# Optimization experiments

Hardware: AMD Instinct MI355X
Metric: run time of the kernel (lower is better)

## Reference

```python
import jax, jax.numpy as jnp
import numpy as np
import math

B, N, E_PER = 128, 512, 2048
D = 16
NUM_REL = 114
NUM_ATTR = 10
LAYERS = 3
RATIO = 0.8
TN = B * N
TE = B * E_PER
NEG_SLOPE = 0.2


def setup_inputs() -> dict:
    key = jax.random.key(0)
    ks = jax.random.split(key, 16)
    x_attr = jax.random.randint(ks[0], (TN,), 0, NUM_ATTR, dtype=jnp.int32)
    # edges constrained within each graph's contiguous block of N nodes
    src = jax.random.randint(ks[1], (B, E_PER), 0, N, dtype=jnp.int32)
    dst = jax.random.randint(ks[2], (B, E_PER), 0, N, dtype=jnp.int32)
    off = (jnp.arange(B, dtype=jnp.int32) * N)[:, None]
    edge_index = jnp.stack([(src + off).reshape(-1), (dst + off).reshape(-1)])
    edge_type = jax.random.randint(ks[3], (TE,), 0, NUM_REL, dtype=jnp.int32)
    emb = jax.random.normal(ks[4], (NUM_ATTR, D)) * 0.3
    gnn_w = jax.random.normal(ks[5], (LAYERS, NUM_REL, D, D)) * (1.0 / np.sqrt(D))
    gnn_q = jax.random.normal(ks[6], (LAYERS, D, 1)) * 0.3
    gnn_k = jax.random.normal(ks[7], (LAYERS, D, 1)) * 0.3
    gnn_b = jnp.zeros((LAYERS, D))
    pool_w = jax.random.normal(ks[8], (LAYERS - 1, D)) * 0.3
    w1 = jax.random.normal(ks[9], (D * LAYERS * 2, 16)) * (1.0 / np.sqrt(D * LAYERS * 2))
    b1 = jnp.zeros((16,))
    w2 = jax.random.normal(ks[10], (16, 4)) * 0.25
    b2 = jnp.zeros((4,))
    w3 = jax.random.normal(ks[11], (4, 1)) * 0.5
    b3 = jnp.zeros((1,))
    return dict(emb=emb, gnn_w=gnn_w, gnn_q=gnn_q, gnn_k=gnn_k, gnn_b=gnn_b,
                pool_w=pool_w, w1=w1, b1=b1, w2=w2, b2=b2, w3=w3, b3=b3,
                x_attr=x_attr, edge_index=edge_index, edge_type=edge_type)


def _rgat_layer(x, src, dst, etype, edge_mask, node_mask, W, q, k, b):
    # PyG RGATConv: heads=1, dim=1, additive-self-attention, across-relation softmax, sum aggr
    w_e = W[etype]                                   # [E, D, D] per-relation gather
    h_s = jnp.einsum('ed,edo->eo', x[src], w_e)      # transformed source (x_j)
    h_t = jnp.einsum('ed,edo->eo', x[dst], w_e)      # transformed target (x_i)
    logit = jax.nn.leaky_relu((h_t @ q + h_s @ k)[:, 0], NEG_SLOPE)  # [E]
    # masked segment softmax over incoming edges of each target node
    m = jax.ops.segment_max(jnp.where(edge_mask, logit, -jnp.inf), dst, num_segments=TN)
    m_e = m[dst]
    ex = jnp.where(edge_mask, jnp.exp(logit - jnp.where(jnp.isfinite(m_e), m_e, 0.0)), 0.0)
    den = jax.ops.segment_sum(ex, dst, num_segments=TN)[dst]
    alpha = ex / jnp.where(den > 0, den, 1.0)
    out = jax.ops.segment_sum(alpha[:, None] * h_s, dst, num_segments=TN) + b
    return jnp.where(node_mask[:, None], jax.nn.relu(out), 0.0)


def reference(emb, gnn_w, gnn_q, gnn_k, gnn_b, pool_w, w1, b1, w2, b2, w3, b3,
              x_attr, edge_index, edge_type):
    src, dst = edge_index[0], edge_index[1]
    x = emb[x_attr]                                  # [TN, D]
    node_mask = jnp.ones((TN,), bool)
    edge_mask = jnp.ones((TE,), bool)
    feats = []
    alive = N
    for l in range(LAYERS):
        x = _rgat_layer(x, src, dst, edge_type, edge_mask, node_mask,
                        gnn_w[l], gnn_q[l], gnn_k[l], gnn_b[l])
        xb = x.reshape(B, N, D)
        mb = node_mask.reshape(B, N)
        cnt = mb.sum(1).astype(x.dtype)[:, None]
        feats.append(xb.sum(1) / cnt)                               # global mean pool
        feats.append(jnp.where(mb[:, :, None], xb, -jnp.inf).max(1))  # global max pool
        if l < LAYERS - 1:
            kk = math.ceil(RATIO * alive)            # static per-graph keep count
            pw = pool_w[l]
            score = jnp.tanh((x @ pw) / jnp.linalg.norm(pw))        # [TN]
            sm = jnp.where(node_mask, score, -jnp.inf).reshape(B, N)
            _, idx = jax.lax.top_k(sm, kk)
            nm = jnp.zeros((B, N), bool).at[jnp.arange(B)[:, None], idx].set(True).reshape(-1)
            x = jnp.where(nm[:, None], x * score[:, None], 0.0)
            node_mask = nm
            edge_mask = edge_mask & nm[src] & nm[dst]
            alive = kk
    g = jnp.concatenate(feats, axis=1)               # [B, 96]
    g = jax.nn.relu(g @ w1 + b1)
    g = jax.nn.relu(g @ w2 + b2)
    return jax.nn.sigmoid(g @ w3 + b3)               # [B, 1]
```

## Files before the change

### kernel.cpp

```cpp
#include <hip/hip_runtime.h>

#define B_ 128
#define NPG 512
#define EPG 2048
#define NREL 114
#define XS 18

__device__ __forceinline__ unsigned fkey(float f){
  unsigned u = __float_as_uint(f);
  return (u & 0x80000000u) ? ~u : (u | 0x80000000u);
}
__device__ __forceinline__ float fdec(unsigned k){
  return (k & 0x80000000u) ? __uint_as_float(k & 0x7FFFFFFFu) : __uint_as_float(~k);
}
__device__ __forceinline__ float dot4f(float4 a, float4 b){
  return a.x*b.x + a.y*b.y + a.z*b.z + a.w*b.w;
}

__device__ __forceinline__ void scan512(int* s_hist, int* s_off, int* s_wt, int tid){
  int lane = tid & 63, wv = tid >> 6;
  int cnt = 0, inc = 0;
  if (wv < 8){
    cnt = s_hist[wv*64 + lane];
    inc = cnt;
    #pragma unroll
    for (int o=1; o<64; o<<=1){ int t=__shfl_up(inc,o); if (lane>=o) inc += t; }
    if (lane==63) s_wt[wv] = inc;
  }
  __syncthreads();
  if (tid < 8){
    int e = 0;
    #pragma unroll
    for (int j=0;j<8;j++) if (j<tid) e += s_wt[j];
    s_wt[8+tid] = e;
  }
  __syncthreads();
  if (wv < 8){
    int base = s_wt[8+wv];
    s_off[wv*64+lane+1] = base + inc;
    s_hist[wv*64+lane]  = base + inc - cnt;
  }
  if (tid==0) s_off[0] = 0;
}

__global__ __launch_bounds__(1024, 4) void k_fused(
    const float* __restrict__ emb, const float* __restrict__ gnn_w,
    const float* __restrict__ gnn_q, const float* __restrict__ gnn_k,
    const float* __restrict__ gnn_b, const float* __restrict__ pool_w,
    const float* __restrict__ w1, const float* __restrict__ b1,
    const float* __restrict__ w2, const float* __restrict__ b2,
    const float* __restrict__ w3, const float* __restrict__ b3,
    const int* __restrict__ xattr, const int* __restrict__ src,
    const int* __restrict__ dst, const int* __restrict__ et,
    float* __restrict__ out)
{
  __shared__ float s_x[NPG*XS];
  __shared__ float s_wq[NREL*XS];
  __shared__ float s_wk[NREL*XS];
  __shared__ unsigned s_epk[EPG+2];
  __shared__ unsigned short s_edst[EPG];
  __shared__ int s_off[NPG+1];
  __shared__ int s_hist[NPG];
  __shared__ unsigned s_keys[NPG];
  __shared__ int s_mask[NPG];
  __shared__ unsigned short s_perm[NPG];
  __shared__ int s_dh[64];
  __shared__ int s_wt[16];
  __shared__ float s_sum[16];
  __shared__ unsigned s_max16[16];
  __shared__ int s_w[16];
  __shared__ float s_feats[96];
  __shared__ float s_h1[16], s_h2[4];

  const int b = blockIdx.x, tid = threadIdx.x;
  const int lane = tid & 63, wv = tid >> 6;
  const int og = tid & 3, grp = tid >> 2;
  const int nb = b*NPG;
  const size_t gb = (size_t)b*EPG;

  if (tid < NPG){
    int a = xattr[nb + tid];
    const float2* e2 = (const float2*)(emb + a*16);
    #pragma unroll
    for (int c=0;c<8;c++) *(float2*)&s_x[tid*XS + 2*c] = e2[c];
    s_mask[tid] = 1;
  }
  for (int i=tid;i<NPG;i+=1024) s_hist[i]=0;
  if (tid<64) s_dh[tid]=0;
  if (tid<2) s_epk[EPG+tid]=0;
  __syncthreads();
  for (int e=tid;e<EPG;e+=1024) atomicAdd(&s_hist[dst[gb+e]-nb], 1);
  __syncthreads();
  scan512(s_hist, s_off, s_wt, tid);
  __syncthreads();
  {
    for (int e=tid;e<EPG;e+=1024){
      int d = dst[gb+e]-nb;
      int p = atomicAdd(&s_hist[d], 1);
      s_epk[p]  = (unsigned)(src[gb+e]-nb) | ((unsigned)et[gb+e]<<16);
      s_edst[p] = (unsigned short)d;
    }
    int mydeg = 0;
    if (tid<NPG){
      mydeg = s_off[tid+1]-s_off[tid]; if (mydeg>63) mydeg=63;
      atomicAdd(&s_dh[mydeg], 1);
    }
    __syncthreads();
    if (tid<64){
      int c = s_dh[tid], inc = c;
      #pragma unroll
      for (int o=1;o<64;o<<=1){ int t=__shfl_up(inc,o); if (tid>=o) inc+=t; }
      s_dh[tid] = inc - c;
    }
    __syncthreads();
    if (tid<NPG){ int p = atomicAdd(&s_dh[mydeg],1); s_perm[p]=(unsigned short)tid; }
  }
  __syncthreads();

  const int cnts[3] = {512, 410, 328};
  const int kks[2]  = {410, 328};

  for (int l=0; l<3; ++l){
    const float* Wl = gnn_w + (size_t)l*NREL*256;
    {
      const float4* q4=(const float4*)(gnn_q+l*16);
      const float4* k4=(const float4*)(gnn_k+l*16);
      float4 q0=q4[0],q1=q4[1],q2=q4[2],q3=q4[3];
      float4 c0=k4[0],c1=k4[1],c2=k4[2],c3=k4[3];
      for (int i=tid;i<NREL*16;i+=1024){
        const float4* wr=(const float4*)(Wl+(size_t)i*16);
        float4 a0=wr[0],a1=wr[1],a2=wr[2],a3=wr[3];
        s_wq[(i>>4)*XS+(i&15)] = dot4f(a0,q0)+dot4f(a1,q1)+dot4f(a2,q2)+dot4f(a3,q3);
        s_wk[(i>>4)*XS+(i&15)] = dot4f(a0,c0)+dot4f(a1,c1)+dot4f(a2,c2)+dot4f(a3,c3);
      }
      if (tid<16){ s_sum[tid]=0.f; s_max16[tid]=0u; }
    }
    __syncthreads();
    float rnorm=0.f; float pw4[4]={0,0,0,0};
    if (l<2){
      float ss=0.f;
      #pragma unroll
      for (int o=0;o<16;o++){ float p=pool_w[l*16+o]; ss+=p*p; }
      rnorm = rsqrtf(ss);
      #pragma unroll
      for (int j=0;j<4;j++) pw4[j]=pool_w[l*16+4*og+j];
    }
    const float* bb = gnn_b + l*16;
    const int nA = s_perm[grp], nB = s_perm[511-grp];
    float zA[4], zB[4];
    auto pm_round = [&](int n, float* z){
      int beg = s_off[n], end = s_off[n+1];
      int alive = s_mask[n];
      float2 xt0 = *(const float2*)&s_x[n*XS+4*og];
      float2 xt1 = *(const float2*)&s_x[n*XS+4*og+2];
      float m = -1e30f;
      float den=0.f, v0=0.f, v1=0.f, v2=0.f, v3=0.f;
      int p = beg;
      unsigned pkA = 0u, pkB = 0u;
      if (p+2 <= end){ pkA = s_epk[p]; pkB = s_epk[p+1]; }
      for (; p+2 <= end; p += 2){
        unsigned pk0 = pkA, pk1 = pkB;
        pkA = s_epk[p+2]; pkB = s_epk[p+3];
        int s0 = pk0 & 0xFFFF, r0 = pk0 >> 16;
        int s1 = pk1 & 0xFFFF, r1 = pk1 >> 16;
        float2 wq00=*(const float2*)&s_wq[r0*XS+4*og];
        float2 wq01=*(const float2*)&s_wq[r0*XS+4*og+2];
        float2 wk00=*(const float2*)&s_wk[r0*XS+4*og];
        float2 wk01=*(const float2*)&s_wk[r0*XS+4*og+2];
        float2 xs00=*(const float2*)&s_x[s0*XS+4*og];
        float2 xs01=*(const float2*)&s_x[s0*XS+4*og+2];
        float a0 = xt0.x*wq00.x + xt0.y*wq00.y + xt1.x*wq01.x + xt1.y*wq01.y
                 + xs00.x*wk00.x + xs00.y*wk00.y + xs01.x*wk01.x + xs01.y*wk01.y;
        float2 wq10=*(const float2*)&s_wq[r1*XS+4*og];
        float2 wq11=*(const float2*)&s_wq[r1*XS+4*og+2];
        float2 wk10=*(const float2*)&s_wk[r1*XS+4*og];
        float2 wk11=*(const float2*)&s_wk[r1*XS+4*og+2];
        float2 xs10=*(const float2*)&s_x[s1*XS+4*og];
        float2 xs11=*(const float2*)&s_x[s1*XS+4*og+2];
        float a1 = xt0.x*wq10.x + xt0.y*wq10.y + xt1.x*wq11.x + xt1.y*wq11.y
                 + xs10.x*wk10.x + xs10.y*wk10.y + xs11.x*wk11.x + xs11.y*wk11.y;
        a0 += __shfl_xor(a0,1); a0 += __shfl_xor(a0,2);
        a1 += __shfl_xor(a1,1); a1 += __shfl_xor(a1,2);
        float lg0 = a0>0.f ? a0 : 0.2f*a0;
        float lg1 = a1>0.f ? a1 : 0.2f*a1;
        const float4* wr0 = (const float4*)(Wl + (size_t)r0*256) + og;
        const float4* wr1 = (const float4*)(Wl + (size_t)r1*256) + og;
        const float* xr0 = &s_x[s0*XS];
        const float* xr1 = &s_x[s1*XS];
        float h00=0.f,h01=0.f,h02=0.f,h03=0.f;
        float h10=0.f,h11=0.f,h12=0.f,h13=0.f;
        #pragma unroll
        for (int d2=0; d2<8; ++d2){
          float2 xa = *(const float2*)&xr0[2*d2];
          float2 xb = *(const float2*)&xr1[2*d2];
          float4 wA0 = wr0[(2*d2)*4], wB0 = wr0[(2*d2+1)*4];
          float4 wA1 = wr1[(2*d2)*4], wB1 = wr1[(2*d2+1)*4];
          h00 += xa.x*wA0.x + xa.y*wB0.x;  h01 += xa.x*wA0.y + xa.y*wB0.y;
          h02 += xa.x*wA0.z + xa.y*wB0.z;  h03 += xa.x*wA0.w + xa.y*wB0.w;
          h10 += xb.x*wA1.x + xb.y*wB1.x;  h11 += xb.x*wA1.y + xb.y*wB1.y;
          h12 += xb.x*wA1.z + xb.y*wB1.z;  h13 += xb.x*wA1.w + xb.y*wB1.w;
        }
        float nm = fmaxf(m, fmaxf(lg0, lg1));
        float sc = __expf(m - nm);
        float e0 = __expf(lg0 - nm);
        float e1 = __expf(lg1 - nm);
        den = den*sc + e0 + e1;
        v0 = v0*sc + e0*h00 + e1*h10;
        v1 = v1*sc + e0*h01 + e1*h11;
        v2 = v2*sc + e0*h02 + e1*h12;
        v3 = v3*sc + e0*h03 + e1*h13;
        m = nm;
      }
      if (p < end){
        unsigned pk = s_epk[p];
        int s = pk & 0xFFFF, r = pk >> 16;
        float2 wq0=*(const float2*)&s_wq[r*XS+4*og];
        float2 wq1=*(const float2*)&s_wq[r*XS+4*og+2];
        float2 wk0=*(const float2*)&s_wk[r*XS+4*og];
        float2 wk1=*(const float2*)&s_wk[r*XS+4*og+2];
        float2 xs0=*(const float2*)&s_x[s*XS+4*og];
        float2 xs1=*(const float2*)&s_x[s*XS+4*og+2];
        float a = xt0.x*wq0.x + xt0.y*wq0.y + xt1.x*wq1.x + xt1.y*wq1.y
                + xs0.x*wk0.x + xs0.y*wk0.y + xs1.x*wk1.x + xs1.y*wk1.y;
        a += __shfl_xor(a,1); a += __shfl_xor(a,2);
        float lg = a>0.f ? a : 0.2f*a;
        const float4* wr = (const float4*)(Wl + (size_t)r*256) + og;
        const float* xr = &s_x[s*XS];
        float h0=0.f,h1=0.f,h2=0.f,h3=0.f;
        #pragma unroll
        for (int d2=0; d2<8; ++d2){
          float2 xs2 = *(const float2*)&xr[2*d2];
          float4 wA = wr[(2*d2)*4];
          float4 wB = wr[(2*d2+1)*4];
          h0 += xs2.x*wA.x + xs2.y*wB.x;
          h1 += xs2.x*wA.y + xs2.y*wB.y;
          h2 += xs2.x*wA.z + xs2.y*wB.z;
          h3 += xs2.x*wA.w + xs2.y*wB.w;
        }
        float nm = fmaxf(m, lg);
        float sc = __expf(m - nm);
        float ex = __expf(lg - nm);
        den = den*sc + ex;
        v0 = v0*sc + ex*h0;
        v1 = v1*sc + ex*h1;
        v2 = v2*sc + ex*h2;
        v3 = v3*sc + ex*h3;
        m = nm;
      }
      float inv = den>0.f ? 1.f/den : 1.f;
      z[0]=v0*inv+bb[4*og+0]; z[1]=v1*inv+bb[4*og+1];
      z[2]=v2*inv+bb[4*og+2]; z[3]=v3*inv+bb[4*og+3];
      #pragma unroll
      for (int j=0;j<4;j++){ if (z[j]<0.f) z[j]=0.f; }
      if (!alive){ z[0]=z[1]=z[2]=z[3]=0.f; }
      #pragma unroll
      for (int j=0;j<4;j++){
        float sv=z[j], mv=z[j];
        #pragma unroll
        for (int off=4; off<64; off<<=1){
          sv += __shfl_xor(sv, off);
          mv = fmaxf(mv, __shfl_xor(mv, off));
        }
        if ((lane>>2)==0){
          atomicAdd(&s_sum[4*og+j], sv);
          atomicMax(&s_max16[4*og+j], __float_as_uint(mv));
        }
      }
      if (l<2){
        float dq = z[0]*pw4[0]+z[1]*pw4[1]+z[2]*pw4[2]+z[3]*pw4[3];
        dq += __shfl_xor(dq,1); dq += __shfl_xor(dq,2);
        if (og==0){
          float sc2 = tanhf(dq*rnorm);
          s_keys[n] = alive ? fkey(sc2) : 0u;
        }
      }
    };
    pm_round(nA, zA);
    pm_round(nB, zB);
    __syncthreads();
    if (tid<16){
      s_feats[l*32+tid]    = s_sum[tid]/(float)cnts[l];
      s_feats[l*32+16+tid] = __uint_as_float(s_max16[tid]);
    }
    if (l==2) break;
    {
      *(float2*)&s_x[nA*XS+4*og]   = make_float2(zA[0],zA[1]);
      *(float2*)&s_x[nA*XS+4*og+2] = make_float2(zA[2],zA[3]);
      *(float2*)&s_x[nB*XS+4*og]   = make_float2(zB[0],zB[1]);
      *(float2*)&s_x[nB*XS+4*og+2] = make_float2(zB[2],zB[3]);
    }
    __syncthreads();
    {
      const int kk = kks[l];
      unsigned kreg[8];
      #pragma unroll
      for (int j=0;j<8;j++) kreg[j] = s_keys[lane + j*64];
      unsigned cur = 0u;
      for (int bit=31; bit>=0; --bit){
        unsigned cand = cur | (1u<<bit);
        int c=0;
        #pragma unroll
        for (int j=0;j<8;j++) c += __popcll(__ballot(kreg[j]>=cand));
        if (c >= kk) cur = cand;
      }
      int cgt=0;
      #pragma unroll
      for (int j=0;j<8;j++) cgt += __popcll(__ballot(kreg[j]>cur));
      int ties = kk - cgt;
      unsigned myk = (tid<NPG) ? s_keys[tid] : 0u;
      bool eq = (tid<NPG) && (myk==cur);
      unsigned long long bal = __ballot(eq);
      int lrank = __popcll(bal & ((1ull<<lane)-1ull));
      if (lane==0) s_w[wv] = __popcll(bal);
      __syncthreads();
      int pre=0;
      #pragma unroll
      for (int w=0; w<16; ++w) if (w<wv) pre += s_w[w];
      int rank = pre + lrank;
      if (tid < NPG){
        bool keep = (myk > cur) || (eq && rank < ties);
        float mult = keep ? fdec(myk) : 0.f;
        #pragma unroll
        for (int c=0;c<8;c++){
          float2 t2 = *(const float2*)&s_x[tid*XS+2*c];
          t2.x *= mult; t2.y *= mult;
          *(float2*)&s_x[tid*XS+2*c] = t2;
        }
        s_mask[tid] = keep ? 1 : 0;
      }
    }
    __syncthreads();
    {
      int ne = s_off[NPG];
      unsigned pk0=0, pk1=0; unsigned short dd0=0, dd1=0; bool k0=false, k1=false;
      if (tid < ne){
        pk0 = s_epk[tid]; dd0 = s_edst[tid];
        k0 = s_mask[pk0 & 0xFFFF] && s_mask[dd0];
      }
      if (tid+1024 < ne){
        pk1 = s_epk[tid+1024]; dd1 = s_edst[tid+1024];
        k1 = s_mask[pk1 & 0xFFFF] && s_mask[dd1];
      }
      __syncthreads();
      for (int i=tid;i<NPG;i+=1024) s_hist[i]=0;
      if (tid<64) s_dh[tid]=0;
      __syncthreads();
      if (k0) atomicAdd(&s_hist[dd0], 1);
      if (k1) atomicAdd(&s_hist[dd1], 1);
      __syncthreads();
      scan512(s_hist, s_off, s_wt, tid);
      __syncthreads();
      if (k0){ int p=atomicAdd(&s_hist[dd0],1); s_epk[p]=pk0; s_edst[p]=dd0; }
      if (k1){ int p=atomicAdd(&s_hist[dd1],1); s_epk[p]=pk1; s_edst[p]=dd1; }
      int mydeg=0;
      if (tid<NPG){
        mydeg = s_off[tid+1]-s_off[tid]; if (mydeg>63) mydeg=63;
        atomicAdd(&s_dh[mydeg], 1);
      }
      __syncthreads();
      if (tid<64){
        int c = s_dh[tid], inc = c;
        #pragma unroll
        for (int o=1;o<64;o<<=1){ int t=__shfl_up(inc,o); if (tid>=o) inc+=t; }
        s_dh[tid] = inc - c;
      }
      __syncthreads();
      if (tid<NPG){ int p = atomicAdd(&s_dh[mydeg],1); s_perm[p]=(unsigned short)tid; }
      __syncthreads();
    }
  }

  __syncthreads();
  if (tid < 16){
    float a = b1[tid];
    for (int i=0;i<96;i++) a += s_feats[i]*w1[i*16+tid];
    s_h1[tid] = a>0.f?a:0.f;
  }
  __syncthreads();
  if (tid < 4){
    float a = b2[tid];
    #pragma unroll
    for (int i=0;i<16;i++) a += s_h1[i]*w2[i*4+tid];
    s_h2[tid] = a>0.f?a:0.f;
  }
  __syncthreads();
  if (tid == 0){
    float z = b3[0];
    #pragma unroll
    for (int i=0;i<4;i++) z += s_h2[i]*w3[i];
    out[b] = 1.f/(1.f+expf(-z));
  }
}

extern "C" void kernel_launch(void* const* d_in, const int* in_sizes, int n_in,
                              void* d_out, int out_size, void* d_ws, size_t ws_size,
                              hipStream_t stream) {
  const float* emb    = (const float*)d_in[0];
  const float* gnn_w  = (const float*)d_in[1];
  const float* gnn_q  = (const float*)d_in[2];
  const float* gnn_k  = (const float*)d_in[3];
  const float* gnn_b  = (const float*)d_in[4];
  const float* pool_w = (const float*)d_in[5];
  const float* w1 = (const float*)d_in[6];
  const float* b1 = (const float*)d_in[7];
  const float* w2 = (const float*)d_in[8];
  const float* b2 = (const float*)d_in[9];
  const float* w3 = (const float*)d_in[10];
  const float* b3 = (const float*)d_in[11];
  const int* xattr = (const int*)d_in[12];
  const int* eidx  = (const int*)d_in[13];
  const int* etype = (const int*)d_in[14];
  const int* src = eidx;
  const int* dst = eidx + (size_t)B_*EPG;

  k_fused<<<B_, 1024, 0, stream>>>(emb, gnn_w, gnn_q, gnn_k, gnn_b, pool_w,
                                   w1, b1, w2, b2, w3, b3,
                                   xattr, src, dst, etype, (float*)d_out);
}
```

Baseline: 100.3 us.

## Replace per-layer edge compaction with a logit penalty for dropped source nodes

Removes the CSR rebuild after each pooling step (edge filtering, histogram, scan, scatter, degree sort) and the s_edst array. Instead, each node row stores a penalty in padding slot 16: 0 if kept, -1e30 if dropped. That penalty is added to the attention logit, so edges from dropped sources get zero softmax weight. Dropped target nodes still iterate their edges, and edges from dropped sources are still processed. This trades several block-wide barriers and atomics for extra edge work in later layers, and the degree-sorted permutation no longer reflects the live edge counts.

```diff
diff --git a/kernel.cpp b/kernel.cpp
--- a/kernel.cpp
+++ b/kernel.cpp
@@ -58,7 +58,6 @@
   __shared__ float s_wq[NREL*XS];
   __shared__ float s_wk[NREL*XS];
   __shared__ unsigned s_epk[EPG+2];
-  __shared__ unsigned short s_edst[EPG];
   __shared__ int s_off[NPG+1];
   __shared__ int s_hist[NPG];
   __shared__ unsigned s_keys[NPG];
@@ -83,6 +82,8 @@
     const float2* e2 = (const float2*)(emb + a*16);
     #pragma unroll
     for (int c=0;c<8;c++) *(float2*)&s_x[tid*XS + 2*c] = e2[c];
+    s_x[tid*XS+16] = 0.f;
+    s_x[tid*XS+17] = 0.f;
     s_mask[tid] = 1;
   }
   for (int i=tid;i<NPG;i+=1024) s_hist[i]=0;
@@ -97,8 +98,7 @@
     for (int e=tid;e<EPG;e+=1024){
       int d = dst[gb+e]-nb;
       int p = atomicAdd(&s_hist[d], 1);
-      s_epk[p]  = (unsigned)(src[gb+e]-nb) | ((unsigned)et[gb+e]<<16);
-      s_edst[p] = (unsigned short)d;
+      s_epk[p] = (unsigned)(src[gb+e]-nb) | ((unsigned)et[gb+e]<<16);
     }
     int mydeg = 0;
     if (tid<NPG){
@@ -163,6 +163,8 @@
         pkA = s_epk[p+2]; pkB = s_epk[p+3];
         int s0 = pk0 & 0xFFFF, r0 = pk0 >> 16;
         int s1 = pk1 & 0xFFFF, r1 = pk1 >> 16;
+        float pen0 = s_x[s0*XS+16];
+        float pen1 = s_x[s1*XS+16];
         float2 wq00=*(const float2*)&s_wq[r0*XS+4*og];
         float2 wq01=*(const float2*)&s_wq[r0*XS+4*og+2];
         float2 wk00=*(const float2*)&s_wk[r0*XS+4*og];
@@ -181,8 +183,8 @@
                  + xs10.x*wk10.x + xs10.y*wk10.y + xs11.x*wk11.x + xs11.y*wk11.y;
         a0 += __shfl_xor(a0,1); a0 += __shfl_xor(a0,2);
         a1 += __shfl_xor(a1,1); a1 += __shfl_xor(a1,2);
-        float lg0 = a0>0.f ? a0 : 0.2f*a0;
-        float lg1 = a1>0.f ? a1 : 0.2f*a1;
+        float lg0 = (a0>0.f ? a0 : 0.2f*a0) + pen0;
+        float lg1 = (a1>0.f ? a1 : 0.2f*a1) + pen1;
         const float4* wr0 = (const float4*)(Wl + (size_t)r0*256) + og;
         const float4* wr1 = (const float4*)(Wl + (size_t)r1*256) + og;
         const float* xr0 = &s_x[s0*XS];
@@ -214,6 +216,7 @@
       if (p < end){
         unsigned pk = s_epk[p];
         int s = pk & 0xFFFF, r = pk >> 16;
+        float pen = s_x[s*XS+16];
         float2 wq0=*(const float2*)&s_wq[r*XS+4*og];
         float2 wq1=*(const float2*)&s_wq[r*XS+4*og+2];
         float2 wk0=*(const float2*)&s_wk[r*XS+4*og];
@@ -223,7 +226,7 @@
         float a = xt0.x*wq0.x + xt0.y*wq0.y + xt1.x*wq1.x + xt1.y*wq1.y
                 + xs0.x*wk0.x + xs0.y*wk0.y + xs1.x*wk1.x + xs1.y*wk1.y;
         a += __shfl_xor(a,1); a += __shfl_xor(a,2);
-        float lg = a>0.f ? a : 0.2f*a;
+        float lg = (a>0.f ? a : 0.2f*a) + pen;
         const float4* wr = (const float4*)(Wl + (size_t)r*256) + og;
         const float* xr = &s_x[s*XS];
         float h0=0.f,h1=0.f,h2=0.f,h3=0.f;
@@ -326,48 +329,11 @@
           t2.x *= mult; t2.y *= mult;
           *(float2*)&s_x[tid*XS+2*c] = t2;
         }
+        s_x[tid*XS+16] = keep ? 0.f : -1e30f;
         s_mask[tid] = keep ? 1 : 0;
       }
     }
     __syncthreads();
-    {
-      int ne = s_off[NPG];
-      unsigned pk0=0, pk1=0; unsigned short dd0=0, dd1=0; bool k0=false, k1=false;
-      if (tid < ne){
-        pk0 = s_epk[tid]; dd0 = s_edst[tid];
-        k0 = s_mask[pk0 & 0xFFFF] && s_mask[dd0];
-      }
-      if (tid+1024 < ne){
-        pk1 = s_epk[tid+1024]; dd1 = s_edst[tid+1024];
-        k1 = s_mask[pk1 & 0xFFFF] && s_mask[dd1];
-      }
-      __syncthreads();
-      for (int i=tid;i<NPG;i+=1024) s_hist[i]=0;
-      if (tid<64) s_dh[tid]=0;
-      __syncthreads();
-      if (k0) atomicAdd(&s_hist[dd0], 1);
-      if (k1) atomicAdd(&s_hist[dd1], 1);
-      __syncthreads();
-      scan512(s_hist, s_off, s_wt, tid);
-      __syncthreads();
-      if (k0){ int p=atomicAdd(&s_hist[dd0],1); s_epk[p]=pk0; s_edst[p]=dd0; }
-      if (k1){ int p=atomicAdd(&s_hist[dd1],1); s_epk[p]=pk1; s_edst[p]=dd1; }
-      int mydeg=0;
-      if (tid<NPG){
-        mydeg = s_off[tid+1]-s_off[tid]; if (mydeg>63) mydeg=63;
-        atomicAdd(&s_dh[mydeg], 1);
-      }
-      __syncthreads();
-      if (tid<64){
-        int c = s_dh[tid], inc = c;
-        #pragma unroll
-        for (int o=1;o<64;o<<=1){ int t=__shfl_up(inc,o); if (tid>=o) inc+=t; }
-        s_dh[tid] = inc - c;
-      }
-      __syncthreads();
-      if (tid<NPG){ int p = atomicAdd(&s_dh[mydeg],1); s_perm[p]=(unsigned short)tid; }
-      __syncthreads();
-    }
   }
 
   __syncthreads();
```

New measurement: 101.4 us. About the same (+1.1%).
